# Optimization experiments

Measured on AMD Instinct MI355X. Metric: run time of the kernel, lower is better.

## Reference

```python
import jax, jax.numpy as jnp
import numpy as np

B, DIM, H, W = 32, 384, 32, 32
ORDER = 5
DIMS = [DIM // 2**i for i in range(ORDER)][::-1]  # [24,48,96,192,384]
SUM_DIMS = sum(DIMS)                               # 744 == 2*DIM - DIMS[0]
SCALE = 1.0 / 3.0
EPS = 1e-5


def setup_inputs() -> dict:
    key = jax.random.key(0)
    ks = jax.random.split(key, 32)

    def n(k, shape, s=0.02):
        return jax.random.normal(k, shape, jnp.float32) * s

    inp = {}
    inp['x'] = jax.random.normal(ks[0], (B, DIM, H, W), jnp.float32)
    # norm1: LayerNorm([dim, H, W]) -> per-element affine
    inp['ln1_w'] = jnp.ones((DIM, H, W), jnp.float32) + n(ks[1], (DIM, H, W))
    inp['ln1_b'] = n(ks[2], (DIM, H, W))
    # gnconv params
    inp['proj_in_w'] = n(ks[3], (2 * DIM, DIM))   # 1x1 conv stored as [O,C]
    inp['proj_in_b'] = n(ks[4], (2 * DIM,))
    inp['dw_w'] = n(ks[5], (SUM_DIMS, 1, 7, 7))   # depthwise 7x7
    inp['dw_b'] = n(ks[6], (SUM_DIMS,))
    for i in range(ORDER - 1):
        inp[f'pw{i}_w'] = n(ks[7 + 2 * i], (DIMS[i + 1], DIMS[i]))
        inp[f'pw{i}_b'] = n(ks[8 + 2 * i], (DIMS[i + 1],))
    inp['proj_out_w'] = n(ks[15], (DIM, DIM))
    inp['proj_out_b'] = n(ks[16], (DIM,))
    # norm2 + MLP
    inp['ln2_w'] = jnp.ones((DIM,), jnp.float32) + n(ks[17], (DIM,))
    inp['ln2_b'] = n(ks[18], (DIM,))
    inp['fc1_w'] = n(ks[19], (4 * DIM, DIM))
    inp['fc1_b'] = n(ks[20], (4 * DIM,))
    inp['fc2_w'] = n(ks[21], (DIM, 4 * DIM))
    inp['fc2_b'] = n(ks[22], (DIM,))
    # layer scales
    inp['gamma1'] = 1e-6 * jnp.ones((DIM,), jnp.float32)
    inp['gamma2'] = 1e-6 * jnp.ones((DIM,), jnp.float32)
    return inp


def _conv1x1(x, w, b):
    # x: [B,C,H,W], w: [O,C] -> [B,O,H,W]
    return jnp.einsum('bchw,oc->bohw', x, w) + b[None, :, None, None]


def _dwconv7(x, w, b):
    y = jax.lax.conv_general_dilated(
        x, w, window_strides=(1, 1), padding=[(3, 3), (3, 3)],
        dimension_numbers=('NCHW', 'OIHW', 'NCHW'),
        feature_group_count=x.shape[1])
    return y + b[None, :, None, None]


def reference(x, ln1_w, ln1_b, proj_in_w, proj_in_b, dw_w, dw_b,
              pw0_w, pw0_b, pw1_w, pw1_b, pw2_w, pw2_b, pw3_w, pw3_b,
              proj_out_w, proj_out_b, ln2_w, ln2_b,
              fc1_w, fc1_b, fc2_w, fc2_b, gamma1, gamma2):
    # ---- norm1: LayerNorm over (C,H,W) jointly ----
    mu = x.mean(axis=(1, 2, 3), keepdims=True)
    var = x.var(axis=(1, 2, 3), keepdims=True)
    h = (x - mu) * jax.lax.rsqrt(var + EPS) * ln1_w[None] + ln1_b[None]

    # ---- gnconv (recursive gated conv) ----
    fused = _conv1x1(h, proj_in_w, proj_in_b)          # [B, 2*DIM, H, W]
    pwa = fused[:, :DIMS[0]]
    abc = fused[:, DIMS[0]:]                            # [B, SUM_DIMS, H, W]
    dw = _dwconv7(abc, dw_w, dw_b) * SCALE
    dw_list = jnp.split(dw, np.cumsum(DIMS)[:-1].tolist(), axis=1)
    y = pwa * dw_list[0]
    for i, (wp, bp) in enumerate([(pw0_w, pw0_b), (pw1_w, pw1_b), (pw2_w, pw2_b), (pw3_w, pw3_b)]):
        y = _conv1x1(y, wp, bp) * dw_list[i + 1]
    y = _conv1x1(y, proj_out_w, proj_out_b)             # [B, DIM, H, W]

    x = x + gamma1[None, :, None, None] * y             # residual 1 (drop_path=0 -> identity)

    # ---- ConvNeXt-style MLP, channels-last ----
    h = jnp.transpose(x, (0, 2, 3, 1))                  # [B,H,W,C]
    mu2 = h.mean(axis=-1, keepdims=True)
    var2 = h.var(axis=-1, keepdims=True)
    h = (h - mu2) * jax.lax.rsqrt(var2 + EPS) * ln2_w + ln2_b
    h = jnp.einsum('bhwc,oc->bhwo', h, fc1_w) + fc1_b
    h = jax.nn.gelu(h, approximate=False)               # torch GELU default = erf
    h = jnp.einsum('bhwc,oc->bhwo', h, fc2_w) + fc2_b
    h = gamma2 * h
    h = jnp.transpose(h, (0, 3, 1, 2))                  # back to NCHW
    return x + h
```

## Files before the change

### kernel.cpp

```cpp
#include <hip/hip_runtime.h>
#include <math.h>

#define HW 1024
#define CDIM 384
#define NB 32
#define MTOT (NB * HW)
#define EPS 1e-5f

typedef unsigned short u16;
typedef short s8v __attribute__((ext_vector_type(8)));
typedef float f4v __attribute__((ext_vector_type(4)));

union U8 { s8v v; u16 u[8]; };

__device__ __forceinline__ float bf2f(u16 u) {
  union { float f; unsigned int i; } x; x.i = ((unsigned int)u) << 16; return x.f;
}
__device__ __forceinline__ u16 f2bf(float f) {
  union { float f; unsigned int i; } x; x.f = f;
  unsigned int r = (x.i + 0x7FFFu + ((x.i >> 16) & 1u)) >> 16;
  return (u16)r;
}
__device__ __forceinline__ float gelu_exact(float v) {
  return 0.5f * v * (1.f + erff(v * 0.70710678118654752f));
}

__device__ __forceinline__ void gload16(const u16* g, u16* l) {
  __builtin_amdgcn_global_load_lds(
      (const __attribute__((address_space(1))) unsigned int*)(unsigned long long)(const void*)g,
      (__attribute__((address_space(3))) unsigned int*)(unsigned int)(unsigned long long)(void*)l,
      16, 0, 0);
}

__global__ __launch_bounds__(256) void k_statsA(const float* __restrict__ x,
                                                float* __restrict__ part) {
  int blk = blockIdx.x;
  const float4* xb = (const float4*)(x + (size_t)blk * 12288);
  float s = 0.f, s2 = 0.f;
  for (int i = threadIdx.x; i < 3072; i += 256) {
    float4 v = xb[i];
    s += v.x + v.y + v.z + v.w;
    s2 += v.x * v.x + v.y * v.y + v.z * v.z + v.w * v.w;
  }
  __shared__ float ls[256], ls2[256];
  ls[threadIdx.x] = s; ls2[threadIdx.x] = s2;
  __syncthreads();
  for (int off = 128; off > 0; off >>= 1) {
    if (threadIdx.x < off) {
      ls[threadIdx.x] += ls[threadIdx.x + off];
      ls2[threadIdx.x] += ls2[threadIdx.x + off];
    }
    __syncthreads();
  }
  if (threadIdx.x == 0) { part[blk * 2] = ls[0]; part[blk * 2 + 1] = ls2[0]; }
}

__global__ void k_statsB(const float* __restrict__ part, float* __restrict__ stats) {
  int b = threadIdx.x;
  if (b >= 32) return;
  float s = 0.f, s2 = 0.f;
  for (int i = 0; i < 32; i++) {
    s += part[(b * 32 + i) * 2];
    s2 += part[(b * 32 + i) * 2 + 1];
  }
  const float inv_n = 1.f / (CDIM * HW);
  float m = s * inv_n;
  stats[b] = m;
  stats[32 + b] = rsqrtf(s2 * inv_n - m * m + EPS);
}

__global__ __launch_bounds__(256) void k_cvtwE(const float* __restrict__ piw,
                                               const float* __restrict__ pow_,
                                               const float* __restrict__ p0w,
                                               const float* __restrict__ p1w,
                                               const float* __restrict__ p2w,
                                               const float* __restrict__ p3w,
                                               u16* __restrict__ dst) {
  int i = blockIdx.x * 256 + threadIdx.x;
  if (i < 294912) dst[i] = f2bf(piw[i]);
  else if (i < 442368) dst[i] = f2bf(pow_[i - 294912]);
  else if (i < 443904) { int j = i - 442368, o = j >> 5, k = j & 31;
    dst[i] = (k < 24) ? f2bf(p0w[o * 24 + k]) : (u16)0; }
  else if (i < 450048) { int j = i - 443904, o = j >> 6, k = j & 63;
    dst[i] = (k < 48) ? f2bf(p1w[o * 48 + k]) : (u16)0; }
  else if (i < 468480) dst[i] = f2bf(p2w[i - 450048]);
  else dst[i] = f2bf(p3w[i - 468480]);
}

__global__ __launch_bounds__(256) void k_cvtwL(const float* __restrict__ fc1,
                                               const float* __restrict__ fc2,
                                               u16* __restrict__ dst) {
  int i = blockIdx.x * 256 + threadIdx.x;
  if (i < 589824) dst[i] = f2bf(fc1[i]);
  else dst[i] = f2bf(fc2[i - 589824]);
}

__global__ __launch_bounds__(256) void k_trln1(const float* __restrict__ x,
                                               const float* __restrict__ lnw,
                                               const float* __restrict__ lnb,
                                               const float* __restrict__ stats,
                                               u16* __restrict__ xn,
                                               u16* __restrict__ hn) {
  int pt = blockIdx.x, ct = blockIdx.y, b = blockIdx.z;
  __shared__ float xs[32][33], hs[32][33];
  float m = stats[b], rs = stats[32 + b];
  int t = threadIdx.x;
  int ci0 = t >> 5, pi = t & 31;
#pragma unroll
  for (int it = 0; it < 4; it++) {
    int ci = ci0 + it * 8;
    int c = ct * 32 + ci;
    size_t src = ((size_t)b * CDIM + c) * HW + pt * 32 + pi;
    size_t wsrc = (size_t)c * HW + pt * 32 + pi;
    float xv = x[src];
    xs[ci][pi] = xv;
    hs[ci][pi] = (xv - m) * rs * lnw[wsrc] + lnb[wsrc];
  }
  __syncthreads();
  int co = t & 31, pr0 = t >> 5;
#pragma unroll
  for (int it = 0; it < 4; it++) {
    int pr = pr0 + it * 8;
    int p = pt * 32 + pr;
    int c = ct * 32 + co;
    size_t dst = ((size_t)b * HW + p) * CDIM + c;
    xn[dst] = f2bf(xs[co][pr]);
    hn[dst] = f2bf(hs[co][pr]);
  }
}

template <int MODE>
__global__ __launch_bounds__(256)
void k_mfma(const u16* __restrict__ A, const u16* __restrict__ Wb,
            const float* __restrict__ bias, void* __restrict__ Out,
            const u16* __restrict__ gate, int gate_off,
            const u16* __restrict__ resbf, const float* __restrict__ gvec,
            int m_base, int K, int O, int OS) {
  __shared__ u16 As[4096];
  __shared__ u16 Bs[4096];
  const int t = threadIdx.x;
  const int m0 = blockIdx.x * 128, o0 = blockIdx.y * 128;
  const int w = t >> 6, l = t & 63;
  const int wm = (w >> 1) * 64, wn = (w & 1) * 64;
  const int lr = l & 15, lk = (l >> 4) * 8;

  const u16* gA = A + (size_t)(m0 + w * 32 + (l >> 2)) * K + (l & 3) * 8;
  const u16* gB = Wb + (size_t)(o0 + w * 32 + (l >> 2)) * K + (l & 3) * 8;
  u16* ldsA0 = As + w * 1024;
  u16* ldsB0 = Bs + w * 1024;

  f4v acc[4][4];
#pragma unroll
  for (int i = 0; i < 4; i++)
#pragma unroll
    for (int j = 0; j < 4; j++) acc[i][j] = {};

  for (int k0 = 0; k0 < K; k0 += 32) {
    gload16(gA + k0, ldsA0);
    gload16(gA + 16 * K + k0, ldsA0 + 512);
    gload16(gB + k0, ldsB0);
    gload16(gB + 16 * K + k0, ldsB0 + 512);
    __syncthreads();
    s8v a[4], b[4];
#pragma unroll
    for (int mi = 0; mi < 4; mi++)
      a[mi] = *(const s8v*)&As[(wm + mi * 16 + lr) * 32 + lk];
#pragma unroll
    for (int fj = 0; fj < 4; fj++)
      b[fj] = *(const s8v*)&Bs[(wn + fj * 16 + lr) * 32 + lk];
#pragma unroll
    for (int mi = 0; mi < 4; mi++)
#pragma unroll
      for (int fj = 0; fj < 4; fj++)
        acc[mi][fj] = __builtin_amdgcn_mfma_f32_16x16x32_bf16(a[mi], b[fj], acc[mi][fj], 0, 0, 0);
    __syncthreads();
  }

  const int orow = (l >> 4) * 4;
#pragma unroll
  for (int mi = 0; mi < 4; mi++) {
    int p = m0 + wm + mi * 16 + orow;
#pragma unroll
    for (int fj = 0; fj < 4; fj++) {
      int o = o0 + wn + fj * 16 + lr;
      if (MODE == 1 && o >= OS) continue;
      float bo = (MODE == 1 && o >= O) ? 0.f : bias[o];
      float gv = (MODE == 2 || MODE == 4) ? gvec[o] : 0.f;
      if (MODE == 4) {
        int gp = m_base + p;
        float4 st;
        float* stp = &st.x;
#pragma unroll
        for (int r = 0; r < 4; r++)
          stp[r] = bf2f(resbf[(size_t)(gp + r) * CDIM + o]) + gv * (acc[mi][fj][r] + bo);
        int bb = gp >> 10, hw = gp & 1023;
        *(float4*)((float*)Out + ((size_t)bb * CDIM + o) * HW + hw) = st;
      } else {
#pragma unroll
        for (int r = 0; r < 4; r++) {
          float val = acc[mi][fj][r] + bo;
          size_t rowi = (size_t)(p + r);
          if (MODE == 0) {
            ((u16*)Out)[rowi * OS + o] = f2bf(val);
          } else if (MODE == 1) {
            float g = (o < O) ? bf2f(gate[rowi * 744 + gate_off + o]) : 0.f;
            ((u16*)Out)[rowi * OS + o] = (o < O) ? f2bf(val * g) : (u16)0;
          } else if (MODE == 2) {
            size_t idx = rowi * CDIM + o;
            ((u16*)Out)[idx] = f2bf(bf2f(resbf[idx]) + gv * val);
          } else if (MODE == 3) {
            ((u16*)Out)[rowi * OS + o] = f2bf(gelu_exact(val));
          }
        }
      }
    }
  }
}

__global__ __launch_bounds__(256) void k_dwconv(const u16* __restrict__ fused,
                                                const float* __restrict__ w,
                                                const float* __restrict__ bias,
                                                u16* __restrict__ dwo) {
  int ys = blockIdx.x;
  int cb = blockIdx.y;
  int b = blockIdx.z;
  __shared__ u16 tile[10][32][64];
  __shared__ float wk[64][49];
  int c0 = cb * 64;
  int t = threadIdx.x;
  for (int i = t; i < 64 * 49; i += 256) {
    int c = i / 49, k = i % 49;
    wk[c][k] = (c0 + c < 744) ? w[(size_t)(c0 + c) * 49 + k] : 0.f;
  }
  int lx = t >> 3, lco = (t & 7) * 8;
  for (int yy = 0; yy < 10; yy++) {
    int y = ys * 4 - 3 + yy;
    U8 v;
    int fch = 24 + c0 + lco;
    if (y >= 0 && y < 32 && fch + 8 <= 768) {
      v.v = *(const s8v*)(fused + ((size_t)b * HW + y * 32 + lx) * 768 + fch);
    } else if (y >= 0 && y < 32) {
      for (int i = 0; i < 8; i++)
        v.u[i] = (fch + i < 768) ? fused[((size_t)b * HW + y * 32 + lx) * 768 + fch + i] : 0;
    } else {
      for (int i = 0; i < 8; i++) v.u[i] = 0;
    }
    *(s8v*)&tile[yy][lx][lco] = v.v;
  }
  __syncthreads();
  int c = t & 63, dy = t >> 6;
  bool valid = (c0 + c) < 744;
  float bv = valid ? bias[c0 + c] : 0.f;
  float acc[32];
#pragma unroll
  for (int x = 0; x < 32; x++) acc[x] = 0.f;
#pragma unroll
  for (int ky = 0; ky < 7; ky++) {
    int yy = dy + ky;
    float r[38];
    r[0] = r[1] = r[2] = 0.f; r[35] = r[36] = r[37] = 0.f;
#pragma unroll
    for (int x = 0; x < 32; x++) r[x + 3] = bf2f(tile[yy][x][c]);
#pragma unroll
    for (int kx = 0; kx < 7; kx++) {
      float wv = wk[c][ky * 7 + kx];
#pragma unroll
      for (int x = 0; x < 32; x++) acc[x] += r[x + kx] * wv;
    }
  }
  if (valid) {
    int yout = ys * 4 + dy;
#pragma unroll
    for (int x = 0; x < 32; x++) {
      dwo[((size_t)b * HW + yout * 32 + x) * 744 + c0 + c] =
          f2bf((acc[x] + bv) * (1.f / 3.f));
    }
  }
}

__global__ __launch_bounds__(256) void k_y0(const u16* __restrict__ fused,
                                            const u16* __restrict__ dwo,
                                            u16* __restrict__ y0) {
  int i = blockIdx.x * 256 + threadIdx.x;
  int p = i >> 5, c = i & 31;
  y0[i] = (c < 24) ? f2bf(bf2f(fused[(size_t)p * 768 + c]) * bf2f(dwo[(size_t)p * 744 + c]))
                   : (u16)0;
}

__global__ __launch_bounds__(256) void k_ln2(const u16* __restrict__ xm,
                                             const float* __restrict__ w,
                                             const float* __restrict__ bb,
                                             u16* __restrict__ outp) {
  int row = blockIdx.x * 4 + (threadIdx.x >> 6);
  int l = threadIdx.x & 63;
  float v[8];
  float s = 0.f, s2 = 0.f;
  if (l < 48) {
    U8 u;
    u.v = *(const s8v*)(xm + (size_t)row * CDIM + l * 8);
#pragma unroll
    for (int i = 0; i < 8; i++) {
      v[i] = bf2f(u.u[i]);
      s += v[i]; s2 += v[i] * v[i];
    }
  }
#pragma unroll
  for (int off = 32; off > 0; off >>= 1) {
    s += __shfl_xor(s, off);
    s2 += __shfl_xor(s2, off);
  }
  const float inv_n = 1.f / CDIM;
  float m = s * inv_n;
  float rs = rsqrtf(s2 * inv_n - m * m + EPS);
  if (l < 48) {
    U8 res;
#pragma unroll
    for (int i = 0; i < 8; i++) {
      int c = l * 8 + i;
      res.u[i] = f2bf((v[i] - m) * rs * w[c] + bb[c]);
    }
    *(s8v*)(outp + (size_t)row * CDIM + l * 8) = res.v;
  }
}

extern "C" void kernel_launch(void* const* d_in, const int* in_sizes, int n_in,
                              void* d_out, int out_size, void* d_ws, size_t ws_size,
                              hipStream_t stream) {
  const float* x          = (const float*)d_in[0];
  const float* ln1_w      = (const float*)d_in[1];
  const float* ln1_b      = (const float*)d_in[2];
  const float* proj_in_w  = (const float*)d_in[3];
  const float* proj_in_b  = (const float*)d_in[4];
  const float* dw_w       = (const float*)d_in[5];
  const float* dw_b       = (const float*)d_in[6];
  const float* pw0_w      = (const float*)d_in[7];
  const float* pw0_b      = (const float*)d_in[8];
  const float* pw1_w      = (const float*)d_in[9];
  const float* pw1_b      = (const float*)d_in[10];
  const float* pw2_w      = (const float*)d_in[11];
  const float* pw2_b      = (const float*)d_in[12];
  const float* pw3_w      = (const float*)d_in[13];
  const float* pw3_b      = (const float*)d_in[14];
  const float* proj_out_w = (const float*)d_in[15];
  const float* proj_out_b = (const float*)d_in[16];
  const float* ln2_w      = (const float*)d_in[17];
  const float* ln2_b      = (const float*)d_in[18];
  const float* fc1_w      = (const float*)d_in[19];
  const float* fc1_b      = (const float*)d_in[20];
  const float* fc2_w      = (const float*)d_in[21];
  const float* fc2_b      = (const float*)d_in[22];
  const float* gamma1     = (const float*)d_in[23];
  const float* gamma2     = (const float*)d_in[24];
  float* out = (float*)d_out;

  const size_t MiB = 1ull << 20;
  char* ws = (char*)d_ws;
  u16* xn   = (u16*)(ws + 0);
  u16* hn   = (u16*)(ws + 24 * MiB);
  u16* fus  = (u16*)(ws + 48 * MiB);
  u16* dw   = (u16*)(ws + 96 * MiB);
  u16* wE   = (u16*)(ws + 142 * MiB + 512 * 1024);
  float* stats = (float*)(ws + 143 * MiB + 768 * 1024);
  float* part  = stats + 64;
  u16* y0 = (u16*)(ws + 24 * MiB);
  u16* y1 = (u16*)(ws + 26 * MiB);
  u16* y2 = (u16*)(ws + 30 * MiB);
  u16* y3 = (u16*)(ws + 36 * MiB);
  u16* y4 = (u16*)(ws + 48 * MiB);
  u16* xmid = (u16*)(ws + 72 * MiB);
  u16* ln2h = (u16*)(ws + 0);
  u16* fc1b = (u16*)(ws + 24 * MiB);
  u16* fc2b = fc1b + 589824;
  u16* h1 = (u16*)(ws + 96 * MiB);

  u16* piw_b = wE;
  u16* pow_b = wE + 294912;
  u16* pw0b  = wE + 442368;
  u16* pw1b  = wE + 443904;
  u16* pw2b  = wE + 450048;
  u16* pw3b  = wE + 468480;

  k_statsA<<<1024, 256, 0, stream>>>(x, part);
  k_statsB<<<1, 64, 0, stream>>>(part, stats);
  k_cvtwE<<<2118, 256, 0, stream>>>(proj_in_w, proj_out_w, pw0_w, pw1_w, pw2_w, pw3_w, wE);
  k_trln1<<<dim3(32, 12, NB), 256, 0, stream>>>(x, ln1_w, ln1_b, stats, xn, hn);
  k_mfma<0><<<dim3(256, 6), 256, 0, stream>>>(hn, piw_b, proj_in_b, fus, nullptr, 0,
                                              nullptr, nullptr, 0, 384, 768, 768);
  k_dwconv<<<dim3(8, 12, NB), 256, 0, stream>>>(fus, dw_w, dw_b, dw);
  k_y0<<<(MTOT * 32) / 256, 256, 0, stream>>>(fus, dw, y0);
  k_mfma<1><<<dim3(256, 1), 256, 0, stream>>>(y0, pw0b, pw0_b, y1, dw, 24, nullptr,
                                              nullptr, 0, 32, 48, 64);
  k_mfma<1><<<dim3(256, 1), 256, 0, stream>>>(y1, pw1b, pw1_b, y2, dw, 72, nullptr,
                                              nullptr, 0, 64, 96, 96);
  k_mfma<1><<<dim3(256, 2), 256, 0, stream>>>(y2, pw2b, pw2_b, y3, dw, 168, nullptr,
                                              nullptr, 0, 96, 192, 192);
  k_mfma<1><<<dim3(256, 3), 256, 0, stream>>>(y3, pw3b, pw3_b, y4, dw, 360, nullptr,
                                              nullptr, 0, 192, 384, 384);
  k_mfma<2><<<dim3(256, 3), 256, 0, stream>>>(y4, pow_b, proj_out_b, xmid, nullptr, 0,
                                              xn, gamma1, 0, 384, 384, 384);
  k_ln2<<<MTOT / 4, 256, 0, stream>>>(xmid, ln2_w, ln2_b, ln2h);
  k_cvtwL<<<4608, 256, 0, stream>>>(fc1_w, fc2_w, fc1b);
  for (int ch = 0; ch < 2; ch++) {
    int m_base = ch * 16384;
    k_mfma<3><<<dim3(128, 12), 256, 0, stream>>>(ln2h + (size_t)m_base * CDIM, fc1b,
                                                 fc1_b, h1, nullptr, 0, nullptr, nullptr,
                                                 0, 384, 1536, 1536);
    k_mfma<4><<<dim3(128, 3), 256, 0, stream>>>(h1, fc2b, fc2_b, out, nullptr, 0, xmid,
                                                gamma2, m_base, 1536, 384, 384);
  }
}
```

Before: 436.8 us.

## Fuse y0 gating into depthwise conv and retile to 32 channels by 8 rows

The depthwise 7x7 conv kernel now also computes y0 (pwa times the first 24 dw channels) in the blocks with channel block 0, which removes the separate k_y0 launch and its reread of dwo. The tiling changes from 64 channels by 4 output rows to 32 channels by 8 output rows, with 14 halo rows loaded per block. This cuts the halo overhead relative to output rows, but each global load now moves 8 bytes instead of 16. The y0 work is concentrated in one channel block, so those blocks do slightly more work than the rest.

```diff
diff --git a/kernel.cpp b/kernel.cpp
--- a/kernel.cpp
+++ b/kernel.cpp
@@ -9,6 +9,7 @@
 
 typedef unsigned short u16;
 typedef short s8v __attribute__((ext_vector_type(8)));
+typedef short s4v __attribute__((ext_vector_type(4)));
 typedef float f4v __attribute__((ext_vector_type(4)));
 
 union U8 { s8v v; u16 u[8]; };
@@ -220,37 +221,33 @@
 __global__ __launch_bounds__(256) void k_dwconv(const u16* __restrict__ fused,
                                                 const float* __restrict__ w,
                                                 const float* __restrict__ bias,
-                                                u16* __restrict__ dwo) {
-  int ys = blockIdx.x;
-  int cb = blockIdx.y;
-  int b = blockIdx.z;
-  __shared__ u16 tile[10][32][64];
-  __shared__ float wk[64][49];
-  int c0 = cb * 64;
-  int t = threadIdx.x;
-  for (int i = t; i < 64 * 49; i += 256) {
+                                                u16* __restrict__ dwo,
+                                                u16* __restrict__ y0) {
+  const int ys = blockIdx.x;
+  const int cb = blockIdx.y;
+  const int b = blockIdx.z;
+  __shared__ u16 tile[14][32][32];
+  __shared__ float wk[32][49];
+  const int c0 = cb * 32;
+  const int t = threadIdx.x;
+  for (int i = t; i < 32 * 49; i += 256) {
     int c = i / 49, k = i % 49;
     wk[c][k] = (c0 + c < 744) ? w[(size_t)(c0 + c) * 49 + k] : 0.f;
   }
-  int lx = t >> 3, lco = (t & 7) * 8;
-  for (int yy = 0; yy < 10; yy++) {
-    int y = ys * 4 - 3 + yy;
-    U8 v;
-    int fch = 24 + c0 + lco;
-    if (y >= 0 && y < 32 && fch + 8 <= 768) {
-      v.v = *(const s8v*)(fused + ((size_t)b * HW + y * 32 + lx) * 768 + fch);
-    } else if (y >= 0 && y < 32) {
-      for (int i = 0; i < 8; i++)
-        v.u[i] = (fch + i < 768) ? fused[((size_t)b * HW + y * 32 + lx) * 768 + fch + i] : 0;
-    } else {
-      for (int i = 0; i < 8; i++) v.u[i] = 0;
-    }
-    *(s8v*)&tile[yy][lx][lco] = v.v;
+  const int lx = t >> 3, cq = (t & 7) * 4;
+  const int fch = 24 + c0 + cq;
+#pragma unroll
+  for (int yy = 0; yy < 14; yy++) {
+    int y = ys * 8 - 3 + yy;
+    s4v v = {0, 0, 0, 0};
+    if (y >= 0 && y < 32 && fch < 768)
+      v = *(const s4v*)(fused + ((size_t)b * HW + y * 32 + lx) * 768 + fch);
+    *(s4v*)&tile[yy][lx][cq] = v;
   }
   __syncthreads();
-  int c = t & 63, dy = t >> 6;
-  bool valid = (c0 + c) < 744;
-  float bv = valid ? bias[c0 + c] : 0.f;
+  const int c = t & 31, dy = t >> 5;
+  const bool valid = (c0 + c) < 744;
+  const float bv = valid ? bias[c0 + c] : 0.f;
   float acc[32];
 #pragma unroll
   for (int x = 0; x < 32; x++) acc[x] = 0.f;
@@ -268,23 +265,22 @@
       for (int x = 0; x < 32; x++) acc[x] += r[x + kx] * wv;
     }
   }
+  const int yout = ys * 8 + dy;
+  const size_t prow = (size_t)b * HW + yout * 32;
   if (valid) {
-    int yout = ys * 4 + dy;
+#pragma unroll
+    for (int x = 0; x < 32; x++)
+      dwo[(prow + x) * 744 + c0 + c] = f2bf((acc[x] + bv) * (1.f / 3.f));
+  }
+  if (cb == 0) {
 #pragma unroll
     for (int x = 0; x < 32; x++) {
-      dwo[((size_t)b * HW + yout * 32 + x) * 744 + c0 + c] =
-          f2bf((acc[x] + bv) * (1.f / 3.f));
-    }
-  }
-}
-
-__global__ __launch_bounds__(256) void k_y0(const u16* __restrict__ fused,
-                                            const u16* __restrict__ dwo,
-                                            u16* __restrict__ y0) {
-  int i = blockIdx.x * 256 + threadIdx.x;
-  int p = i >> 5, c = i & 31;
-  y0[i] = (c < 24) ? f2bf(bf2f(fused[(size_t)p * 768 + c]) * bf2f(dwo[(size_t)p * 744 + c]))
-                   : (u16)0;
+      u16 o = 0;
+      if (c < 24)
+        o = f2bf(bf2f(fused[(prow + x) * 768 + c]) * ((acc[x] + bv) * (1.f / 3.f)));
+      y0[(prow + x) * 32 + c] = o;
+    }
+  }
 }
 
 __global__ __launch_bounds__(256) void k_ln2(const u16* __restrict__ xm,
@@ -386,8 +382,7 @@
   k_trln1<<<dim3(32, 12, NB), 256, 0, stream>>>(x, ln1_w, ln1_b, stats, xn, hn);
   k_mfma<0><<<dim3(256, 6), 256, 0, stream>>>(hn, piw_b, proj_in_b, fus, nullptr, 0,
                                               nullptr, nullptr, 0, 384, 768, 768);
-  k_dwconv<<<dim3(8, 12, NB), 256, 0, stream>>>(fus, dw_w, dw_b, dw);
-  k_y0<<<(MTOT * 32) / 256, 256, 0, stream>>>(fus, dw, y0);
+  k_dwconv<<<dim3(4, 24, NB), 256, 0, stream>>>(fus, dw_w, dw_b, dw, y0);
   k_mfma<1><<<dim3(256, 1), 256, 0, stream>>>(y0, pw0b, pw0_b, y1, dw, 24, nullptr,
                                               nullptr, 0, 32, 48, 64);
   k_mfma<1><<<dim3(256, 1), 256, 0, stream>>>(y1, pw1b, pw1_b, y2, dw, 72, nullptr,
```

Result: no change. 440.4 us (+0.8%).
